# Optimization experiments

Hardware: AMD Instinct MI355X
Metric: run time of the kernel (lower is better)

Reference implementation:

```python
import jax, jax.numpy as jnp
import numpy as np

B, T, C = 512, 256, 384  # batch, seq (<= block_size 256), n_embed
HEAD = 64


def setup_inputs() -> dict:
    key = jax.random.key(0)
    k1, k2, k3, k4 = jax.random.split(key, 4)
    scale = 1.0 / np.sqrt(C)
    return {
        "x": jax.random.normal(k1, (B, T, C), dtype=jnp.float32),
        "Wq": jax.random.normal(k2, (C, HEAD), dtype=jnp.float32) * scale,
        "Wk": jax.random.normal(k3, (C, HEAD), dtype=jnp.float32) * scale,
        "Wv": jax.random.normal(k4, (C, HEAD), dtype=jnp.float32) * scale,
    }


def reference(x, Wq, Wk, Wv):
    # Single causal self-attention head (dropout in eval mode / identity).
    _, T_, C_ = x.shape
    q = x @ Wq  # [B,T,H]
    k = x @ Wk  # [B,T,H]
    v = x @ Wv  # [B,T,H]
    # NOTE: original scales by n_embed**-0.5 (C), not head_size**-0.5.
    wei = jnp.einsum('bth,bsh->bts', q, k) * (C_ ** -0.5)  # [B,T,T]
    causal = jnp.tril(jnp.ones((T_, T_), dtype=bool))
    wei = jnp.where(causal, wei, -jnp.inf)
    wei = jax.nn.softmax(wei, axis=-1)
    return jnp.einsum('bts,bsh->bth', wei, v)  # [B,T,H]
```

## Files before the change

### kernel.cpp

```cpp
#include <hip/hip_runtime.h>

#define B_ 512
#define T_ 256
#define C_ 384
#define H_ 64

typedef __attribute__((ext_vector_type(8))) short bf16x8;
typedef __attribute__((ext_vector_type(4))) float f32x4;

__device__ __forceinline__ short f2bf(float f) {
    unsigned u = __float_as_uint(f);
    u += 0x7fffu + ((u >> 16) & 1u);
    return (short)(u >> 16);
}

__device__ __forceinline__ bf16x8 pack8(float4 a, float4 b) {
    bf16x8 r;
    r[0] = f2bf(a.x); r[1] = f2bf(a.y); r[2] = f2bf(a.z); r[3] = f2bf(a.w);
    r[4] = f2bf(b.x); r[5] = f2bf(b.y); r[6] = f2bf(b.z); r[7] = f2bf(b.w);
    return r;
}

__global__ void pack_w_kernel(const float* __restrict__ Wq, const float* __restrict__ Wk,
                              const float* __restrict__ Wv, short* __restrict__ wp) {
    int p = blockIdx.x * 256 + threadIdx.x;
    if (p >= 12 * 12 * 512) return;
    int j    = p & 7;
    int lane = (p >> 3) & 63;
    int pc   = p >> 9;
    int ct = pc % 12, ks = pc / 12;
    int n  = ct * 16 + (lane & 15);
    int kk = ks * 32 + (lane >> 4) * 8 + j;
    const float* src = (n < 64) ? Wq : ((n < 128) ? Wk : Wv);
    wp[p] = f2bf(src[kk * 64 + (n & 63)]);
}

__global__ __launch_bounds__(1024, 4) void fused_kernel(
    const float* __restrict__ x, const short* __restrict__ wp,
    float* __restrict__ out) {
    __shared__ short Ks[32 * 512];
    __shared__ short Vs[32 * 512];
    __shared__ short Pb[16][16 * 40];

    const int b = blockIdx.x;
    const int tid = threadIdx.x;
    const int w = tid >> 6, lane = tid & 63;
    const int cl = lane & 15, quad = lane >> 4;

    const int rg = (w & 12) | ((w & 3) ^ (w >> 2));
    const int base = rg << 4;

    const float* xb = x + (long)b * (T_ * C_);
    const float4* xr = (const float4*)(xb + (long)(base + cl) * C_) + quad * 2;

    f32x4 acc[12];
    #pragma unroll
    for (int ct = 0; ct < 12; ct++) {
        f32x4 z = {0.f, 0.f, 0.f, 0.f};
        acc[ct] = z;
    }

    float4 xa[3][2];
    xa[0][0] = xr[0]; xa[0][1] = xr[1];
    xa[1][0] = xr[8]; xa[1][1] = xr[9];
    const short* wl = wp + lane * 8;
    #pragma unroll
    for (int ks = 0; ks < 12; ks++) {
        if (ks < 10) {
            xa[(ks + 2) % 3][0] = xr[(ks + 2) * 8];
            xa[(ks + 2) % 3][1] = xr[(ks + 2) * 8 + 1];
        }
        bf16x8 a = pack8(xa[ks % 3][0], xa[ks % 3][1]);
        const short* wk = wl + ks * 6144;
        #pragma unroll
        for (int ct = 0; ct < 12; ct++) {
            bf16x8 bf = *(const bf16x8*)(wk + ct * 512);
            acc[ct] = __builtin_amdgcn_mfma_f32_16x16x32_bf16(a, bf, acc[ct], 0, 0, 0);
        }
    }

    const int tb = base + quad * 4;
    #pragma unroll
    for (int ct = 4; ct < 8; ct++) {
        const int h = (ct - 4) * 16 + cl;
        const int kk = h >> 5, hq = (h & 31) >> 3, j = h & 7;
        #pragma unroll
        for (int r = 0; r < 4; r++) {
            const int t = tb + r;
            Ks[((t >> 4) * 2 + kk) * 512 + ((t & 15) + 16 * hq) * 8 + j] =
                f2bf(acc[ct][r]);
        }
    }
    #pragma unroll
    for (int ct = 8; ct < 12; ct++) {
        const int ht = ct - 8;
        #pragma unroll
        for (int r = 0; r < 4; r++) {
            const int t = tb + r;
            Vs[((t >> 5) * 4 + ht) * 512 + (cl + 16 * ((t >> 3) & 3)) * 8 + (t & 7)] =
                f2bf(acc[ct][r]);
        }
    }

    short* pb = Pb[w];
    bf16x8 qf[2];
    #pragma unroll
    for (int kk = 0; kk < 2; kk++) {
        #pragma unroll
        for (int cth = 0; cth < 2; cth++) {
            const int ct = kk * 2 + cth;
            #pragma unroll
            for (int r = 0; r < 4; r++)
                pb[(quad * 4 + r) * 40 + cth * 16 + cl] = f2bf(acc[ct][r]);
        }
        __builtin_amdgcn_wave_barrier();
        qf[kk] = *(const bf16x8*)(pb + cl * 40 + quad * 8);
        __builtin_amdgcn_wave_barrier();
    }

    __syncthreads();

    const float scale2 = 0.05103103630798287f * 1.4426950408889634f;

    const bf16x8 qf0 = qf[0];
    const bf16x8 qf1 = qf[1];

    f32x4 sacc[16];
    #pragma unroll
    for (int st = 0; st < 16; st++) {
        if (st > rg) continue;
        bf16x8 k0 = *(const bf16x8*)(Ks + (st * 2 + 0) * 512 + lane * 8);
        bf16x8 k1 = *(const bf16x8*)(Ks + (st * 2 + 1) * 512 + lane * 8);
        f32x4 z = {0.f, 0.f, 0.f, 0.f};
        f32x4 t = __builtin_amdgcn_mfma_f32_16x16x32_bf16(qf0, k0, z, 0, 0, 0);
        t = __builtin_amdgcn_mfma_f32_16x16x32_bf16(qf1, k1, t, 0, 0, 0);
        sacc[st] = t;
    }

    float m4[4] = {-3e38f, -3e38f, -3e38f, -3e38f};
    #pragma unroll
    for (int st = 0; st < 16; st++) {
        if (st > rg) continue;
        #pragma unroll
        for (int r = 0; r < 4; r++) {
            float sv = sacc[st][r] * scale2;
            if (st * 16 + cl > base + quad * 4 + r) sv = -1e30f;
            sacc[st][r] = sv;
            m4[r] = fmaxf(m4[r], sv);
        }
    }
    #pragma unroll
    for (int d = 1; d < 16; d <<= 1)
        #pragma unroll
        for (int r = 0; r < 4; r++)
            m4[r] = fmaxf(m4[r], __shfl_xor(m4[r], d));

    float l4[4] = {0.f, 0.f, 0.f, 0.f};
    #pragma unroll
    for (int st = 0; st < 16; st++) {
        if (st > rg) continue;
        #pragma unroll
        for (int r = 0; r < 4; r++) {
            float pv = exp2f(sacc[st][r] - m4[r]);
            sacc[st][r] = pv;
            l4[r] += pv;
        }
    }
    #pragma unroll
    for (int d = 1; d < 16; d <<= 1)
        #pragma unroll
        for (int r = 0; r < 4; r++)
            l4[r] += __shfl_xor(l4[r], d);

    f32x4 oacc[4];
    #pragma unroll
    for (int ht = 0; ht < 4; ht++) {
        f32x4 z = {0.f, 0.f, 0.f, 0.f};
        oacc[ht] = z;
    }
    #pragma unroll
    for (int c = 0; c < 8; c++) {
        if (c > (rg >> 1)) continue;
        #pragma unroll
        for (int half = 0; half < 2; half++) {
            const int st = c * 2 + half;
            #pragma unroll
            for (int r = 0; r < 4; r++) {
                short pv = (st <= rg) ? f2bf(sacc[st][r]) : (short)0;
                pb[(quad * 4 + r) * 40 + half * 16 + cl] = pv;
            }
        }
        __builtin_amdgcn_wave_barrier();
        const bf16x8 pa = *(const bf16x8*)(pb + cl * 40 + quad * 8);
        #pragma unroll
        for (int ht = 0; ht < 4; ht++) {
            const bf16x8 vf = *(const bf16x8*)(Vs + (c * 4 + ht) * 512 + lane * 8);
            oacc[ht] = __builtin_amdgcn_mfma_f32_16x16x32_bf16(pa, vf, oacc[ht], 0, 0, 0);
        }
        __builtin_amdgcn_wave_barrier();
    }

    #pragma unroll
    for (int r = 0; r < 4; r++) {
        const float inv = 1.0f / l4[r];
        float* op = out + (long)(b * T_ + base + quad * 4 + r) * H_ + cl;
        #pragma unroll
        for (int ht = 0; ht < 4; ht++)
            op[ht * 16] = oacc[ht][r] * inv;
    }
}

extern "C" void kernel_launch(void* const* d_in, const int* in_sizes, int n_in,
                              void* d_out, int out_size, void* d_ws, size_t ws_size,
                              hipStream_t stream) {
    const float* x  = (const float*)d_in[0];
    const float* Wq = (const float*)d_in[1];
    const float* Wk = (const float*)d_in[2];
    const float* Wv = (const float*)d_in[3];
    float* out = (float*)d_out;

    short* wp = (short*)d_ws;

    pack_w_kernel<<<288, 256, 0, stream>>>(Wq, Wk, Wv, wp);
    fused_kernel<<<B_, 1024, 0, stream>>>(x, wp, out);
}
```

Baseline: 331.5 us.

## Stage x through double-buffered LDS and tile QKV projection 4x3 per wave

The QKV projection now stages bf16-converted x chunks through swizzled, double-buffered LDS. Each wave computes a 64-row by 48-column register tile, so one A fragment is reused across three B fragments and one B fragment across four row tiles, cutting global weight fetches per wave. Q is written to LDS in MFMA fragment layout and read back by the row-group wave, which replaces the old per-wave Pb transpose. The cost is more LDS (about 116 KB), six extra block barriers in the projection loop, and a Q store/reload round trip.

Measured after the change: 312.0 us. 1.06x faster.

```diff
diff --git a/kernel.cpp b/kernel.cpp
--- a/kernel.cpp
+++ b/kernel.cpp
@@ -14,11 +14,11 @@
     return (short)(u >> 16);
 }
 
-__device__ __forceinline__ bf16x8 pack8(float4 a, float4 b) {
-    bf16x8 r;
-    r[0] = f2bf(a.x); r[1] = f2bf(a.y); r[2] = f2bf(a.z); r[3] = f2bf(a.w);
-    r[4] = f2bf(b.x); r[5] = f2bf(b.y); r[6] = f2bf(b.z); r[7] = f2bf(b.w);
-    return r;
+__device__ __forceinline__ unsigned long long pack4(float4 a) {
+    return  (unsigned long long)(unsigned short)f2bf(a.x)
+         | ((unsigned long long)(unsigned short)f2bf(a.y) << 16)
+         | ((unsigned long long)(unsigned short)f2bf(a.z) << 32)
+         | ((unsigned long long)(unsigned short)f2bf(a.w) << 48);
 }
 
 __global__ void pack_w_kernel(const float* __restrict__ Wq, const float* __restrict__ Wk,
@@ -38,92 +38,143 @@
 __global__ __launch_bounds__(1024, 4) void fused_kernel(
     const float* __restrict__ x, const short* __restrict__ wp,
     float* __restrict__ out) {
-    __shared__ short Ks[32 * 512];
-    __shared__ short Vs[32 * 512];
-    __shared__ short Pb[16][16 * 40];
+    __shared__ char lds_raw[118784];
+    short* Qs = (short*)lds_raw;
+    short* Ks = (short*)(lds_raw + 32768);
+    short* Vs = (short*)(lds_raw + 65536);
+    short* Pb = (short*)(lds_raw + 98304);
 
     const int b = blockIdx.x;
     const int tid = threadIdx.x;
     const int w = tid >> 6, lane = tid & 63;
     const int cl = lane & 15, quad = lane >> 4;
 
+    const float* xb = x + (long)b * (T_ * C_);
+    const float4* xb4 = (const float4*)xb;
+
+    const int srow = w * 16 + quad;
+    const unsigned st_even = (unsigned)(w * 2048 + quad * 128)
+                           + (((unsigned)(cl >> 1) ^ (unsigned)quad) << 4)
+                           + (unsigned)(lane & 1) * 8;
+    const unsigned st_odd = st_even ^ 64u;
+
+    const int rtb = (w & 3) * 4;
+    const int ctb = (w >> 2) * 3;
+    const unsigned abase = (unsigned)((rtb * 16 + cl) * 128)
+                         + (((unsigned)quad ^ (unsigned)(cl & 7)) << 4);
+
+    const short* wlB = wp + ctb * 512 + lane * 8;
+
+    f32x4 acc[4][3];
+    #pragma unroll
+    for (int i = 0; i < 4; i++)
+        #pragma unroll
+        for (int j = 0; j < 3; j++) {
+            f32x4 z = {0.f, 0.f, 0.f, 0.f};
+            acc[i][j] = z;
+        }
+
+    {
+        float4 sv[4];
+        #pragma unroll
+        for (int i = 0; i < 4; i++)
+            sv[i] = xb4[(srow + i * 4) * 96 + cl];
+        #pragma unroll
+        for (int i = 0; i < 4; i++) {
+            unsigned a = ((i & 1) ? st_odd : st_even) + (unsigned)i * 512u;
+            *(unsigned long long*)(lds_raw + a) = pack4(sv[i]);
+        }
+    }
+    __syncthreads();
+
+    for (int c = 0; c < 6; ++c) {
+        bf16x8 bfr[2][3];
+        #pragma unroll
+        for (int kl = 0; kl < 2; kl++) {
+            const short* wk = wlB + (c * 2 + kl) * 6144;
+            #pragma unroll
+            for (int j = 0; j < 3; j++)
+                bfr[kl][j] = *(const bf16x8*)(wk + j * 512);
+        }
+
+        float4 sv[4];
+        if (c < 5) {
+            #pragma unroll
+            for (int i = 0; i < 4; i++)
+                sv[i] = xb4[(srow + i * 4) * 96 + (c + 1) * 16 + cl];
+        }
+
+        const char* buf = lds_raw + (c & 1) * 32768;
+        #pragma unroll
+        for (int kl = 0; kl < 2; kl++) {
+            bf16x8 af[4];
+            #pragma unroll
+            for (int i = 0; i < 4; i++)
+                af[i] = *(const bf16x8*)(buf +
+                    ((abase + (unsigned)i * 2048u) ^ (kl ? 64u : 0u)));
+            #pragma unroll
+            for (int i = 0; i < 4; i++)
+                #pragma unroll
+                for (int j = 0; j < 3; j++)
+                    acc[i][j] = __builtin_amdgcn_mfma_f32_16x16x32_bf16(
+                        af[i], bfr[kl][j], acc[i][j], 0, 0, 0);
+        }
+
+        if (c < 5) {
+            char* nbuf = lds_raw + ((c + 1) & 1) * 32768;
+            #pragma unroll
+            for (int i = 0; i < 4; i++) {
+                unsigned a = ((i & 1) ? st_odd : st_even) + (unsigned)i * 512u;
+                *(unsigned long long*)(nbuf + a) = pack4(sv[i]);
+            }
+        }
+        __syncthreads();
+    }
+
+    #pragma unroll
+    for (int j = 0; j < 3; j++) {
+        const int ct = ctb + j;
+        if (ct < 4) {
+            const int h = ct * 16 + cl;
+            const int kk = h >> 5, hq = (h >> 3) & 3, jj = h & 7;
+            #pragma unroll
+            for (int i = 0; i < 4; i++)
+                #pragma unroll
+                for (int r = 0; r < 4; r++)
+                    Qs[((rtb + i) * 2 + kk) * 512 + ((quad * 4 + r) + 16 * hq) * 8 + jj] =
+                        f2bf(acc[i][j][r]);
+        } else if (ct < 8) {
+            const int h = (ct - 4) * 16 + cl;
+            const int kk = h >> 5, hq = (h >> 3) & 3, jj = h & 7;
+            #pragma unroll
+            for (int i = 0; i < 4; i++)
+                #pragma unroll
+                for (int r = 0; r < 4; r++)
+                    Ks[((rtb + i) * 2 + kk) * 512 + ((quad * 4 + r) + 16 * hq) * 8 + jj] =
+                        f2bf(acc[i][j][r]);
+        } else {
+            const int ht = ct - 8;
+            #pragma unroll
+            for (int i = 0; i < 4; i++)
+                #pragma unroll
+                for (int r = 0; r < 4; r++) {
+                    const int t = (rtb + i) * 16 + quad * 4 + r;
+                    Vs[((t >> 5) * 4 + ht) * 512 + (cl + 16 * ((t >> 3) & 3)) * 8 + (t & 7)] =
+                        f2bf(acc[i][j][r]);
+                }
+        }
+    }
+
+    __syncthreads();
+
+    const float scale2 = 0.05103103630798287f * 1.4426950408889634f;
+
     const int rg = (w & 12) | ((w & 3) ^ (w >> 2));
     const int base = rg << 4;
-
-    const float* xb = x + (long)b * (T_ * C_);
-    const float4* xr = (const float4*)(xb + (long)(base + cl) * C_) + quad * 2;
-
-    f32x4 acc[12];
-    #pragma unroll
-    for (int ct = 0; ct < 12; ct++) {
-        f32x4 z = {0.f, 0.f, 0.f, 0.f};
-        acc[ct] = z;
-    }
-
-    float4 xa[3][2];
-    xa[0][0] = xr[0]; xa[0][1] = xr[1];
-    xa[1][0] = xr[8]; xa[1][1] = xr[9];
-    const short* wl = wp + lane * 8;
-    #pragma unroll
-    for (int ks = 0; ks < 12; ks++) {
-        if (ks < 10) {
-            xa[(ks + 2) % 3][0] = xr[(ks + 2) * 8];
-            xa[(ks + 2) % 3][1] = xr[(ks + 2) * 8 + 1];
-        }
-        bf16x8 a = pack8(xa[ks % 3][0], xa[ks % 3][1]);
-        const short* wk = wl + ks * 6144;
-        #pragma unroll
-        for (int ct = 0; ct < 12; ct++) {
-            bf16x8 bf = *(const bf16x8*)(wk + ct * 512);
-            acc[ct] = __builtin_amdgcn_mfma_f32_16x16x32_bf16(a, bf, acc[ct], 0, 0, 0);
-        }
-    }
-
-    const int tb = base + quad * 4;
-    #pragma unroll
-    for (int ct = 4; ct < 8; ct++) {
-        const int h = (ct - 4) * 16 + cl;
-        const int kk = h >> 5, hq = (h & 31) >> 3, j = h & 7;
-        #pragma unroll
-        for (int r = 0; r < 4; r++) {
-            const int t = tb + r;
-            Ks[((t >> 4) * 2 + kk) * 512 + ((t & 15) + 16 * hq) * 8 + j] =
-                f2bf(acc[ct][r]);
-        }
-    }
-    #pragma unroll
-    for (int ct = 8; ct < 12; ct++) {
-        const int ht = ct - 8;
-        #pragma unroll
-        for (int r = 0; r < 4; r++) {
-            const int t = tb + r;
-            Vs[((t >> 5) * 4 + ht) * 512 + (cl + 16 * ((t >> 3) & 3)) * 8 + (t & 7)] =
-                f2bf(acc[ct][r]);
-        }
-    }
-
-    short* pb = Pb[w];
-    bf16x8 qf[2];
-    #pragma unroll
-    for (int kk = 0; kk < 2; kk++) {
-        #pragma unroll
-        for (int cth = 0; cth < 2; cth++) {
-            const int ct = kk * 2 + cth;
-            #pragma unroll
-            for (int r = 0; r < 4; r++)
-                pb[(quad * 4 + r) * 40 + cth * 16 + cl] = f2bf(acc[ct][r]);
-        }
-        __builtin_amdgcn_wave_barrier();
-        qf[kk] = *(const bf16x8*)(pb + cl * 40 + quad * 8);
-        __builtin_amdgcn_wave_barrier();
-    }
-
-    __syncthreads();
-
-    const float scale2 = 0.05103103630798287f * 1.4426950408889634f;
-
-    const bf16x8 qf0 = qf[0];
-    const bf16x8 qf1 = qf[1];
+    short* pb = Pb + w * 640;
+
+    const bf16x8 qf0 = *(const bf16x8*)(Qs + (rg * 2 + 0) * 512 + lane * 8);
+    const bf16x8 qf1 = *(const bf16x8*)(Qs + (rg * 2 + 1) * 512 + lane * 8);
 
     f32x4 sacc[16];
     #pragma unroll
@@ -179,11 +230,11 @@
         oacc[ht] = z;
     }
     #pragma unroll
-    for (int c = 0; c < 8; c++) {
-        if (c > (rg >> 1)) continue;
+    for (int cc = 0; cc < 8; cc++) {
+        if (cc > (rg >> 1)) continue;
         #pragma unroll
         for (int half = 0; half < 2; half++) {
-            const int st = c * 2 + half;
+            const int st = cc * 2 + half;
             #pragma unroll
             for (int r = 0; r < 4; r++) {
                 short pv = (st <= rg) ? f2bf(sacc[st][r]) : (short)0;
@@ -194,7 +245,7 @@
         const bf16x8 pa = *(const bf16x8*)(pb + cl * 40 + quad * 8);
         #pragma unroll
         for (int ht = 0; ht < 4; ht++) {
-            const bf16x8 vf = *(const bf16x8*)(Vs + (c * 4 + ht) * 512 + lane * 8);
+            const bf16x8 vf = *(const bf16x8*)(Vs + (cc * 4 + ht) * 512 + lane * 8);
             oacc[ht] = __builtin_amdgcn_mfma_f32_16x16x32_bf16(pa, vf, oacc[ht], 0, 0, 0);
         }
         __builtin_amdgcn_wave_barrier();
```
